# Optimization experiments

Hardware: AMD Instinct MI355X
Metric: run time of the kernel (lower is better)

## Reference

```python
import jax, jax.numpy as jnp
import numpy as np

D = 1024   # cfg.hid (downscaled from 8192)
M = 20000  # cfg.mem_c // 2 (downscaled)
B, LQ = 4, 8
PLAST_S = 0.05
IMPORTANCE = 1.0


def mha_shared_kv(q, kv_k, kv_v, Wi, bi, Wo, bo, nheads):
    """torch nn.MultiheadAttention (batch_first) with batch-shared K/V.
    q: [B,Lq,D]; kv_k/kv_v: [Lk,D] shared across batch (avoids the .repeat()
    materialization in the original torch code while computing identical math)."""
    dh = D // nheads
    Wq, Wk, Wv = jnp.split(Wi, 3, axis=0)
    bq, bk, bv = jnp.split(bi, 3)
    qp = (jnp.einsum('bqd,ed->bqe', q, Wq) + bq) * (dh ** -0.5)
    kp = kv_k @ Wk.T + bk              # [Lk,D]
    vp = kv_v @ Wv.T + bv              # [Lk,D]
    qh = qp.reshape(q.shape[0], q.shape[1], nheads, dh)      # [B,Lq,h,dh]
    kh = kp.reshape(kp.shape[0], nheads, dh)                 # [Lk,h,dh]
    vh = vp.reshape(vp.shape[0], nheads, dh)                 # [Lk,h,dh]
    scores = jnp.einsum('bqhd,khd->bhqk', qh, kh)            # [B,h,Lq,Lk]
    attn = jax.nn.softmax(scores, axis=-1)
    ctx = jnp.einsum('bhqk,khd->bqhd', attn, vh)
    ctx = ctx.reshape(q.shape[0], q.shape[1], D)
    return ctx @ Wo.T + bo


def setup_inputs() -> dict:
    key = jax.random.key(0)
    ks = jax.random.split(key, 16)
    s = 0.02
    return {
        'q':    jax.random.normal(ks[0], (B, LQ, D), jnp.float32),
        'data': jax.random.normal(ks[1], (B, D), jnp.float32),
        'ek':   jax.random.normal(ks[2], (M, D), jnp.float32),
        'ev':   jax.random.normal(ks[3], (M, D), jnp.float32),
        'sk':   jax.random.normal(ks[4], (M, D), jnp.float32),
        'sv':   jax.random.normal(ks[5], (M, D), jnp.float32),
        'wm':   jax.random.normal(ks[6], (10, D), jnp.float32),
        'Wi_e': jax.random.normal(ks[7], (3 * D, D), jnp.float32) * s,
        'bi_e': jnp.zeros((3 * D,), jnp.float32),
        'Wo_e': jax.random.normal(ks[8], (D, D), jnp.float32) * s,
        'bo_e': jnp.zeros((D,), jnp.float32),
        'Wi_s': jax.random.normal(ks[9], (3 * D, D), jnp.float32) * s,
        'bi_s': jnp.zeros((3 * D,), jnp.float32),
        'Wo_s': jax.random.normal(ks[10], (D, D), jnp.float32) * s,
        'bo_s': jnp.zeros((D,), jnp.float32),
        'Wi_w': jax.random.normal(ks[11], (3 * D, D), jnp.float32) * s,
        'bi_w': jnp.zeros((3 * D,), jnp.float32),
        'Wo_w': jax.random.normal(ks[12], (D, D), jnp.float32) * s,
        'bo_w': jnp.zeros((D,), jnp.float32),
        'Wrp':  jax.random.normal(ks[13], (D, 3 * D), jnp.float32) * s,
        'brp':  jnp.zeros((D,), jnp.float32),
        'eu':   jnp.zeros((M,), jnp.float32),
    }


def reference(q, data, ek, ev, sk, sv, wm,
              Wi_e, bi_e, Wo_e, bo_e,
              Wi_s, bi_s, Wo_s, bo_s,
              Wi_w, bi_w, Wo_w, bo_w,
              Wrp, brp, eu):
    # ---- NeuroMemory.read ----
    e_r = mha_shared_kv(q, ek, ev, Wi_e, bi_e, Wo_e, bo_e, 16)
    s_r = mha_shared_kv(q, sk, sv, Wi_s, bi_s, Wo_s, bo_s, 16)
    w_r = mha_shared_kv(q, wm, wm, Wi_w, bi_w, Wo_w, bo_w, 8)
    read_out = jnp.concatenate([e_r, s_r, w_r], axis=-1) @ Wrp.T + brp  # [B,Lq,D]

    # ---- NeuroMemory.write (episodic, Hebbian plasticity update) ----
    scores = data @ ek.T                       # [B,M]
    probs = jax.nn.softmax(scores, axis=-1)    # [B,M]
    upd = probs * (PLAST_S * IMPORTANCE)       # [B,M]
    u = upd.mean(axis=0)[:, None]              # [M,1] (batch-mean update strength)
    d = data.mean(axis=0)[None, :]             # [1,D]
    new_ek = ek * (1.0 - u) + d * u            # [M,D]
    new_ev = ev * (1.0 - u) + d * u            # [M,D]
    new_eu = eu * 0.99 + jax.lax.stop_gradient(probs.sum(axis=0))  # [M]
    return (read_out, new_ek, new_ev, new_eu)
```

## Files before the change

### kernel.cpp

```cpp
#include <hip/hip_runtime.h>
#include <hip/hip_fp16.h>
#include <hip/hip_bf16.h>
#include <cstdint>
#include <cstddef>

#define D_HID 1024
#define MEM_M 20000
#define NBATCH 4
#define BL 32
#define NROWS 512
#define SROWS_E 516
#define SROWS_S 512
#define BK 32
#define LDT 40
#define PV_NC 20

typedef __attribute__((ext_vector_type(8))) short short8;
typedef __attribute__((ext_vector_type(4))) float f32x4;
typedef __attribute__((ext_vector_type(16))) float f32x16;
typedef __attribute__((ext_vector_type(4))) unsigned short us4;

__device__ inline ushort f2bf(float f) {
    __hip_bfloat16 b = __float2bfloat16(f);
    return *reinterpret_cast<ushort*>(&b);
}
__device__ inline float h2f(ushort u) {
    __half h; *reinterpret_cast<ushort*>(&h) = u; return __half2float(h);
}

__device__ __forceinline__ void block_sync_lds() {
    asm volatile("s_waitcnt lgkmcnt(0)" ::: "memory");
    __builtin_amdgcn_s_barrier();
}

struct SkDesc  { const float* A; const float* B; int K; int M; };
struct SkDescs { SkDesc d[5]; };
struct RdDesc  { const float* bias; float* dst; int M; int ldc; float alpha; };
struct RdDescs { RdDesc d[5]; };

__device__ __forceinline__ void skinny_body(const SkDesc dd, float* __restrict__ part,
                                            int gk, int k0, int n0, int tid)
{
    __shared__ float As[32][132];
    __shared__ float Bs[64][129];
    const int K = dd.K, M = dd.M;
    {
        const int r = tid >> 3, cbl = (tid & 7) * 16;
        if (r < M) {
            const float* src = dd.A + (size_t)r * K + k0 + cbl;
            #pragma unroll
            for (int i = 0; i < 4; ++i) {
                const float4 v = *(const float4*)(src + i * 4);
                As[r][cbl + i * 4 + 0] = v.x; As[r][cbl + i * 4 + 1] = v.y;
                As[r][cbl + i * 4 + 2] = v.z; As[r][cbl + i * 4 + 3] = v.w;
            }
        } else {
            #pragma unroll
            for (int i = 0; i < 16; ++i) As[r][cbl + i] = 0.f;
        }
    }
    {
        const int r = tid >> 2, cbl = (tid & 3) * 32;
        const float* src = dd.B + (size_t)(n0 + r) * K + k0 + cbl;
        #pragma unroll
        for (int i = 0; i < 8; ++i) {
            const float4 v = *(const float4*)(src + i * 4);
            Bs[r][cbl + i * 4 + 0] = v.x; Bs[r][cbl + i * 4 + 1] = v.y;
            Bs[r][cbl + i * 4 + 2] = v.z; Bs[r][cbl + i * 4 + 3] = v.w;
        }
    }
    __syncthreads();
    const int n = tid & 63, mg = tid >> 6;
    float acc[8];
    #pragma unroll
    for (int i = 0; i < 8; ++i) acc[i] = 0.f;
    #pragma unroll 4
    for (int k = 0; k < 128; k += 4) {
        const float b0 = Bs[n][k + 0], b1 = Bs[n][k + 1];
        const float b2 = Bs[n][k + 2], b3 = Bs[n][k + 3];
        #pragma unroll
        for (int i = 0; i < 8; ++i) {
            const float4 a = *(const float4*)&As[mg * 8 + i][k];
            acc[i] = fmaf(a.x, b0, fmaf(a.y, b1, fmaf(a.z, b2, fmaf(a.w, b3, acc[i]))));
        }
    }
    #pragma unroll
    for (int i = 0; i < 8; ++i)
        part[((size_t)gk * 32 + mg * 8 + i) * 1024 + n0 + n] = acc[i];
}

__global__ __launch_bounds__(256)
void k_skinny(SkDescs ds, float* __restrict__ part)
{
    skinny_body(ds.d[blockIdx.z], part,
                blockIdx.z * gridDim.y + blockIdx.y,
                blockIdx.y * 128, blockIdx.x * 64, threadIdx.x);
}

__global__ __launch_bounds__(256)
void k_head(SkDescs ds, float* __restrict__ part,
            const float* __restrict__ ek, const float* __restrict__ sk,
            ushort* __restrict__ kvb)
{
    const int bx = blockIdx.x;
    const int tid = threadIdx.x;
    if (bx < 640) {
        const int g = bx >> 7;
        const int rem = bx & 127;
        const int kc = rem >> 4;
        const int n0 = (rem & 15) * 64;
        skinny_body(ds.d[g], part, g * 8 + kc, kc * 128, n0, tid);
    } else {
        const size_t nchunks = (size_t)2 * MEM_M * D_HID / 8;
        for (size_t i = (size_t)(bx - 640) * 256 + tid; i < nchunks;
             i += (size_t)1408 * 256) {
            const size_t base = i * 8;
            const float* src = (base < (size_t)MEM_M * D_HID)
                             ? (ek + base) : (sk + base - (size_t)MEM_M * D_HID);
            const float4 v0 = *(const float4*)(src);
            const float4 v1 = *(const float4*)(src + 4);
            alignas(16) ushort o[8];
            o[0] = f2bf(v0.x); o[1] = f2bf(v0.y); o[2] = f2bf(v0.z); o[3] = f2bf(v0.w);
            o[4] = f2bf(v1.x); o[5] = f2bf(v1.y); o[6] = f2bf(v1.z); o[7] = f2bf(v1.w);
            *(short8*)(kvb + base) = *(const short8*)o;
        }
    }
}

__global__ __launch_bounds__(256)
void k_skred(RdDescs ds, const float* __restrict__ part, int nkc)
{
    const int g = blockIdx.y;
    const int m = blockIdx.x;
    const RdDesc dd = ds.d[g];
    if (m >= dd.M) return;
    const int c = threadIdx.x * 4;
    float4 s = make_float4(0.f, 0.f, 0.f, 0.f);
    for (int kc = 0; kc < nkc; ++kc) {
        const float4 v = *(const float4*)&part[((size_t)(g * nkc + kc) * 32 + m) * 1024 + c];
        s.x += v.x; s.y += v.y; s.z += v.z; s.w += v.w;
    }
    const float4 b = *(const float4*)(dd.bias + c);
    float4 o;
    o.x = (s.x + b.x) * dd.alpha; o.y = (s.y + b.y) * dd.alpha;
    o.z = (s.z + b.z) * dd.alpha; o.w = (s.w + b.w) * dd.alpha;
    *(float4*)(dd.dst + (size_t)m * dd.ldc + c) = o;
}

__global__ __launch_bounds__(256)
void mfma_scores(const ushort* __restrict__ A_e, const ushort* __restrict__ ekb,
                 const ushort* __restrict__ A_s, const ushort* __restrict__ skb,
                 __half* __restrict__ S_e, __half* __restrict__ S_s,
                 const float* __restrict__ c0_e, const float* __restrict__ c0_s)
{
    __shared__ ushort As[2][128][LDT];
    __shared__ ushort Bs[2][128][LDT];
    const int tid = threadIdx.x;
    const int i = blockIdx.x + 9 * blockIdx.y;
    const int xcd = i & 7, idx = i >> 3;
    const int wg = (xcd < 5 ? xcd * 177 : 885 + (xcd - 5) * 176) + idx;
    const int mi = wg % 9, nbk = wg / 9;
    const int bank = (mi >= 5);
    const int m0 = (bank ? (mi - 5) : mi) * 128;
    const int n0 = nbk * 128;
    const ushort* __restrict__ A = bank ? A_s : A_e;
    const ushort* __restrict__ B = bank ? skb : ekb;
    __half* __restrict__ S = bank ? S_s : S_e;
    const float* __restrict__ c0 = bank ? c0_s : c0_e;
    const int Mreal = bank ? SROWS_S : SROWS_E;

    const int wid = tid >> 6, lane = tid & 63;
    const int wr = (wid >> 1) * 64, wc = (wid & 1) * 64;
    const int l31 = lane & 31, l2 = lane >> 5;

    const int srow = tid >> 1;
    const int ac = (tid & 1) * 16;
    int gbrow = n0 + srow; if (gbrow > MEM_M - 1) gbrow = MEM_M - 1;
    const ushort* Ap = A + (size_t)(m0 + srow) * 1024 + ac;
    const ushort* Bp = B + (size_t)gbrow * 1024 + ac;

    f32x16 acc[2][2];
    #pragma unroll
    for (int fm = 0; fm < 2; ++fm)
        #pragma unroll
        for (int fn = 0; fn < 2; ++fn)
            #pragma unroll
            for (int r = 0; r < 16; ++r) acc[fm][fn][r] = 0.f;

    auto MF = [&](int bu) {
        short8 a[2][2], b[2][2];
        #pragma unroll
        for (int f = 0; f < 2; ++f)
            #pragma unroll
            for (int kh = 0; kh < 2; ++kh) {
                a[f][kh] = *(const short8*)&As[bu][wr + f * 32 + l31][kh * 16 + l2 * 8];
                b[f][kh] = *(const short8*)&Bs[bu][wc + f * 32 + l31][kh * 16 + l2 * 8];
            }
        #pragma unroll
        for (int fm = 0; fm < 2; ++fm)
            #pragma unroll
            for (int fn = 0; fn < 2; ++fn)
                #pragma unroll
                for (int kh = 0; kh < 2; ++kh)
                    acc[fm][fn] = __builtin_amdgcn_mfma_f32_32x32x16_bf16(
                        a[fm][kh], b[fn][kh], acc[fm][fn], 0, 0, 0);
    };

    short8 a00, a01, b00, b01;
    short8 a10, a11, b10, b11;

#define SC_LOAD0(KT) { a00 = *(const short8*)(Ap + (KT)); a01 = *(const short8*)(Ap + (KT) + 8); \
                       b00 = *(const short8*)(Bp + (KT)); b01 = *(const short8*)(Bp + (KT) + 8); }
#define SC_LOAD1(KT) { a10 = *(const short8*)(Ap + (KT)); a11 = *(const short8*)(Ap + (KT) + 8); \
                       b10 = *(const short8*)(Bp + (KT)); b11 = *(const short8*)(Bp + (KT) + 8); }
#define SC_STORE0(BU) { *(short8*)&As[BU][srow][ac] = a00; *(short8*)&As[BU][srow][ac + 8] = a01; \
                        *(short8*)&Bs[BU][srow][ac] = b00; *(short8*)&Bs[BU][srow][ac + 8] = b01; }
#define SC_STORE1(BU) { *(short8*)&As[BU][srow][ac] = a10; *(short8*)&As[BU][srow][ac + 8] = a11; \
                        *(short8*)&Bs[BU][srow][ac] = b10; *(short8*)&Bs[BU][srow][ac + 8] = b11; }

    SC_LOAD0(0);
    SC_LOAD1(32);
    SC_STORE0(0);
    block_sync_lds();
    for (int it = 0; it < 16; ++it) {
        const int kt = it * 64;
        if (it < 15) SC_LOAD0(kt + 64);
        MF(0);
        SC_STORE1(1);
        block_sync_lds();
        if (it < 15) SC_LOAD1(kt + 96);
        MF(1);
        if (it < 15) SC_STORE0(0);
        block_sync_lds();
    }
#undef SC_LOAD0
#undef SC_LOAD1
#undef SC_STORE0
#undef SC_STORE1

    #pragma unroll
    for (int fm = 0; fm < 2; ++fm) {
        #pragma unroll
        for (int fn = 0; fn < 2; ++fn) {
            #pragma unroll
            for (int r = 0; r < 16; ++r) {
                const int row = m0 + wr + fm * 32 + (r & 3) + 8 * (r >> 2) + 4 * l2;
                if (row >= Mreal) continue;
                const int col = n0 + wc + fn * 32 + l31;
                if (col < MEM_M)
                    S[(size_t)row * MEM_M + col] = __float2half(acc[fm][fn][r] + c0[row]);
            }
        }
    }
}

__global__ __launch_bounds__(256, 3)
void mfma_pv(const ushort* __restrict__ P_e, const ushort* __restrict__ P_s,
             const float* __restrict__ ev, const float* __restrict__ sv,
             float* __restrict__ part)
{
    __shared__ ushort As[2][128][LDT];
    __shared__ ushort Bs[2][128][LDT];
    const int tid = threadIdx.x;
    const int z = blockIdx.z;
    const int bank = (z >= PV_NC), c = bank ? (z - PV_NC) : z;
    const ushort* __restrict__ P = bank ? P_s : P_e;
    const float* __restrict__ V = bank ? sv : ev;
    const int m0 = blockIdx.y * 128, n0 = blockIdx.x * 128;
    const int ks0 = (c * 625) / PV_NC, ks1 = ((c + 1) * 625) / PV_NC;
    const int wid = tid >> 6, lane = tid & 63;
    const int wr = (wid >> 1) * 64, wc = (wid & 1) * 64;
    const int l31 = lane & 31, l2 = lane >> 5;
    const int kb = (tid & 7) * 4, nb2 = (tid >> 3) * 4;
    const int srow = tid >> 1, ac = (tid & 1) * 16;
    const ushort* Pp = P + (size_t)(m0 + srow) * MEM_M + ac;

    f32x16 acc[2][2];
    #pragma unroll
    for (int fm = 0; fm < 2; ++fm)
        #pragma unroll
        for (int fn = 0; fn < 2; ++fn)
            #pragma unroll
            for (int r = 0; r < 16; ++r) acc[fm][fn][r] = 0.f;

    auto MF = [&](int bu) {
        short8 a[2][2], b[2][2];
        #pragma unroll
        for (int f = 0; f < 2; ++f)
            #pragma unroll
            for (int kh = 0; kh < 2; ++kh) {
                a[f][kh] = *(const short8*)&As[bu][wr + f * 32 + l31][kh * 16 + l2 * 8];
                b[f][kh] = *(const short8*)&Bs[bu][wc + f * 32 + l31][kh * 16 + l2 * 8];
            }
        #pragma unroll
        for (int fm = 0; fm < 2; ++fm)
            #pragma unroll
            for (int fn = 0; fn < 2; ++fn)
                #pragma unroll
                for (int kh = 0; kh < 2; ++kh)
                    acc[fm][fn] = __builtin_amdgcn_mfma_f32_32x32x16_bf16(
                        a[fm][kh], b[fn][kh], acc[fm][fn], 0, 0, 0);
    };

    short8 pa0, pa1;
    float4 q0[4], q1[4];

#define PV_PLOAD(T) { const int kt = (T) * 32; \
    pa0 = *(const short8*)(Pp + kt); pa1 = *(const short8*)(Pp + kt + 8); }
#define PV_VLOAD(QQ, T) { const int kt = (T) * 32; \
    QQ[0] = *(const float4*)(V + (size_t)(kt + kb + 0) * 1024 + n0 + nb2); \
    QQ[1] = *(const float4*)(V + (size_t)(kt + kb + 1) * 1024 + n0 + nb2); \
    QQ[2] = *(const float4*)(V + (size_t)(kt + kb + 2) * 1024 + n0 + nb2); \
    QQ[3] = *(const float4*)(V + (size_t)(kt + kb + 3) * 1024 + n0 + nb2); }
#define PV_STORE(BU, QQ) { \
    *(short8*)&As[BU][srow][ac] = pa0; *(short8*)&As[BU][srow][ac + 8] = pa1; \
    us4 w; \
    w.x = f2bf(QQ[0].x); w.y = f2bf(QQ[1].x); w.z = f2bf(QQ[2].x); w.w = f2bf(QQ[3].x); \
    *(us4*)&Bs[BU][nb2 + 0][kb] = w; \
    w.x = f2bf(QQ[0].y); w.y = f2bf(QQ[1].y); w.z = f2bf(QQ[2].y); w.w = f2bf(QQ[3].y); \
    *(us4*)&Bs[BU][nb2 + 1][kb] = w; \
    w.x = f2bf(QQ[0].z); w.y = f2bf(QQ[1].z); w.z = f2bf(QQ[2].z); w.w = f2bf(QQ[3].z); \
    *(us4*)&Bs[BU][nb2 + 2][kb] = w; \
    w.x = f2bf(QQ[0].w); w.y = f2bf(QQ[1].w); w.z = f2bf(QQ[2].w); w.w = f2bf(QQ[3].w); \
    *(us4*)&Bs[BU][nb2 + 3][kb] = w; }

    PV_PLOAD(ks0);
    PV_VLOAD(q0, ks0);
    PV_STORE(0, q0);
    if (ks0 + 1 < ks1) PV_VLOAD(q1, ks0 + 1);
    block_sync_lds();
    for (int t = ks0; t < ks1; t += 2) {
        if (t + 1 < ks1) PV_PLOAD(t + 1);
        if (t + 2 < ks1) PV_VLOAD(q0, t + 2);
        MF(0);
        if (t + 1 < ks1) PV_STORE(1, q1);
        block_sync_lds();
        if (t + 1 < ks1) {
            if (t + 2 < ks1) PV_PLOAD(t + 2);
            if (t + 3 < ks1) PV_VLOAD(q1, t + 3);
            MF(1);
            if (t + 2 < ks1) PV_STORE(0, q0);
            block_sync_lds();
        }
    }
#undef PV_PLOAD
#undef PV_VLOAD
#undef PV_STORE

    float* __restrict__ po = part + (size_t)z * NROWS * 1024;
    #pragma unroll
    for (int fm = 0; fm < 2; ++fm)
        #pragma unroll
        for (int fn = 0; fn < 2; ++fn)
            #pragma unroll
            for (int r = 0; r < 16; ++r) {
                const int row = m0 + wr + fm * 32 + (r & 3) + 8 * (r >> 2) + 4 * l2;
                const int col = n0 + wc + fn * 32 + l31;
                po[(size_t)row * 1024 + col] = acc[fm][fn][r];
            }
}

__global__ __launch_bounds__(256)
void k_T(const float* __restrict__ qp,
         const float* __restrict__ Wi_e, const float* __restrict__ bi_e,
         const float* __restrict__ Wi_s, const float* __restrict__ bi_s,
         ushort* __restrict__ A_e, float* __restrict__ c0_e,
         ushort* __restrict__ A_s, float* __restrict__ c0_s,
         const float* __restrict__ data, float* __restrict__ dmean)
{
    const int bq = blockIdx.x;
    const int tid = threadIdx.x;
    if (bq >= 128) {
        if (bq < 252) {
            const int row = SROWS_E + (bq - 128);
            us4 z4; z4.x = 0; z4.y = 0; z4.z = 0; z4.w = 0;
            *(us4*)(A_e + (size_t)row * 1024 + tid * 4) = z4;
        } else {
            for (int t = tid; t < D_HID; t += 256) {
                float s = 0.f;
                #pragma unroll
                for (int b = 0; b < NBATCH; ++b) s += data[b * D_HID + t];
                dmean[t] = 0.25f * s;
                #pragma unroll
                for (int b = 0; b < NBATCH; ++b)
                    A_e[(size_t)(NROWS + b) * 1024 + t] = f2bf(data[b * D_HID + t]);
            }
            if (tid < NBATCH) c0_e[NROWS + tid] = 0.f;
        }
        return;
    }
    const int bank = bq >> 6;
    const int h = (bq >> 2) & 15;
    const int q4 = bq & 3;
    const float* qpB = qp + (size_t)bank * BL * D_HID;
    const float* Wk = (bank ? Wi_s : Wi_e) + (size_t)D_HID * D_HID;
    const float* bk = (bank ? bi_s : bi_e) + D_HID;
    ushort* T  = bank ? A_s : A_e;
    float* c0 = bank ? c0_s : c0_e;

    __shared__ float qs[32][64];
    for (int i = tid; i < 32 * 64; i += 256) {
        const int r = i >> 6, j = i & 63;
        qs[r][j] = qpB[(size_t)r * D_HID + h * 64 + j];
    }
    __syncthreads();
    const int e = q4 * 256 + tid;
    float acc[32];
    #pragma unroll
    for (int r = 0; r < 32; ++r) acc[r] = 0.f;
    for (int j = 0; j < 64; ++j) {
        const float w = Wk[(size_t)(h * 64 + j) * D_HID + e];
        #pragma unroll
        for (int r = 0; r < 32; ++r) acc[r] = fmaf(qs[r][j], w, acc[r]);
    }
    #pragma unroll
    for (int r = 0; r < 32; ++r) T[(size_t)(r * 16 + h) * 1024 + e] = f2bf(acc[r]);
    if (q4 == 0 && tid < 32) {
        float s = 0.f;
        for (int j = 0; j < 64; ++j) s += qs[tid][j] * bk[h * 64 + j];
        c0[tid * 16 + h] = s;
    }
}

__global__ __launch_bounds__(256)
void k_softmax(__half* __restrict__ S_e, __half* __restrict__ S_s,
               float* __restrict__ mrow, float* __restrict__ lrow)
{
    const int row = blockIdx.x;
    ushort* p = (row < SROWS_E) ? (ushort*)(S_e + (size_t)row * MEM_M)
                                : (ushort*)(S_s + (size_t)(row - SROWS_E) * MEM_M);
    const bool conv = (row < SROWS_E) ? (row < NROWS) : true;
    __shared__ float red_m[256];
    __shared__ float red_l[256];
    const int tid = threadIdx.x;
    float m = -3.0e38f, l = 0.f;
    for (int c = tid; c < MEM_M / 8; c += 256) {
        alignas(16) ushort t[8];
        *(short8*)t = *(const short8*)(p + c * 8);
        float v[8];
        #pragma unroll
        for (int j = 0; j < 8; ++j) v[j] = h2f(t[j]);
        float cm = v[0];
        #pragma unroll
        for (int j = 1; j < 8; ++j) cm = fmaxf(cm, v[j]);
        const float nm = fmaxf(m, cm);
        float s = 0.f;
        #pragma unroll
        for (int j = 0; j < 8; ++j) s += __expf(v[j] - nm);
        l = l * __expf(m - nm) + s;
        m = nm;
    }
    red_m[tid] = m; red_l[tid] = l; __syncthreads();
    for (int s = 128; s > 0; s >>= 1) {
        if (tid < s) {
            const float m2 = fmaxf(red_m[tid], red_m[tid + s]);
            red_l[tid] = red_l[tid] * __expf(red_m[tid] - m2)
                       + red_l[tid + s] * __expf(red_m[tid + s] - m2);
            red_m[tid] = m2;
        }
        __syncthreads();
    }
    const float rm = red_m[0];
    if (conv) {
        for (int c = tid; c < MEM_M / 8; c += 256) {
            alignas(16) ushort t[8];
            *(short8*)t = *(const short8*)(p + c * 8);
            alignas(16) ushort o[8];
            #pragma unroll
            for (int j = 0; j < 8; ++j) o[j] = f2bf(__expf(h2f(t[j]) - rm));
            *(short8*)(p + c * 8) = *(const short8*)o;
        }
    }
    if (tid == 0) { mrow[row] = rm; lrow[row] = red_l[0]; }
}

__global__ __launch_bounds__(256)
void k_uk(const __half* __restrict__ S_e,
          const float* __restrict__ mrow, const float* __restrict__ lrow,
          const float* __restrict__ eu,
          float* __restrict__ u, float* __restrict__ out_eu)
{
    const int k = blockIdx.x * 256 + threadIdx.x;
    if (k >= MEM_M) return;
    float sp = 0.f;
    #pragma unroll
    for (int b = 0; b < NBATCH; ++b) {
        const int row = NROWS + b;
        sp += __expf(__half2float(S_e[(size_t)row * MEM_M + k]) - mrow[row]) / lrow[row];
    }
    u[k] = 0.05f * 0.25f * sp;
    out_eu[k] = eu[k] * 0.99f + sp;
}

__global__ __launch_bounds__(256)
void k_pvred_upd(const float* __restrict__ part, const float* __restrict__ lrow,
                 float* __restrict__ R,
                 const float* __restrict__ ev, const float* __restrict__ u,
                 const float* __restrict__ dmean, float* __restrict__ out_ev)
{
    const int tid = threadIdx.x;
    if (blockIdx.x < 1024) {
        const size_t perb4 = (size_t)NROWS * 1024 / 4;
        const size_t i = (size_t)blockIdx.x * 256 + tid;
        const int bank = i >= perb4;
        const size_t off4 = i - (size_t)bank * perb4;
        const int m = (int)(off4 >> 8);
        const float inv = 1.f / lrow[bank ? (SROWS_E + m) : m];
        const float4* p = (const float4*)part + (size_t)bank * PV_NC * perb4 + off4;
        float4 s = make_float4(0.f, 0.f, 0.f, 0.f);
        #pragma unroll
        for (int c = 0; c < PV_NC; ++c) {
            const float4 v = p[(size_t)c * perb4];
            s.x += v.x; s.y += v.y; s.z += v.z; s.w += v.w;
        }
        s.x *= inv; s.y *= inv; s.z *= inv; s.w *= inv;
        ((float4*)R)[i] = s;
    } else {
        const int bid = blockIdx.x - 1024;
        const size_t n4 = (size_t)MEM_M * D_HID / 4;
        for (size_t i = (size_t)bid * 256 + tid; i < n4; i += (size_t)1024 * 256) {
            const int k = (int)(i >> 8);
            const int c = (int)(i & 255);
            const float uk = u[k];
            const float om = 1.f - uk;
            const float4 dd = ((const float4*)dmean)[c];
            const float4 b = ((const float4*)ev)[i];
            float4 ob;
            ob.x = b.x * om + dd.x * uk; ob.y = b.y * om + dd.y * uk;
            ob.z = b.z * om + dd.z * uk; ob.w = b.w * om + dd.w * uk;
            ((float4*)out_ev)[i] = ob;
        }
    }
}

__global__ __launch_bounds__(256)
void k_tail(const float* __restrict__ R,
            const float* __restrict__ Wi_e, const float* __restrict__ bi_e,
            const float* __restrict__ Wi_s, const float* __restrict__ bi_s,
            float* __restrict__ ctx,
            const float* __restrict__ qp, const float* __restrict__ kpw,
            const float* __restrict__ vpw,
            const float* __restrict__ ek, const float* __restrict__ u,
            const float* __restrict__ dmean, float* __restrict__ out_ek)
{
    __shared__ float sm[12384];
    const int tid = threadIdx.x;
    const int bx = blockIdx.x;
    if (bx < 32) {
        const int bank = bx >> 4;
        const int h = bx & 15;
        const float* Rb = R + (size_t)bank * NROWS * D_HID;
        const float* Wv = (bank ? Wi_s : Wi_e) + (size_t)2 * D_HID * D_HID;
        const float* bv = (bank ? bi_s : bi_e) + 2 * D_HID;
        float* cb = ctx + (size_t)bank * BL * D_HID;
        float (*Rs)[129] = (float(*)[129])sm;
        float (*Ws)[129] = (float(*)[129])(sm + 32 * 129);
        const int j = tid & 63;
        const int g = tid >> 6;
        float acc[8];
        #pragma unroll
        for (int i = 0; i < 8; ++i) acc[i] = 0.f;
        for (int ec = 0; ec < D_HID; ec += 128) {
            for (int i = tid; i < 32 * 128; i += 256) {
                const int r = i >> 7, e = i & 127;
                Rs[r][e] = Rb[(size_t)(r * 16 + h) * D_HID + ec + e];
            }
            for (int i = tid; i < 64 * 128; i += 256) {
                const int r = i >> 7, e = i & 127;
                Ws[r][e] = Wv[(size_t)(h * 64 + r) * D_HID + ec + e];
            }
            __syncthreads();
            for (int e = 0; e < 128; ++e) {
                const float w = Ws[j][e];
                #pragma unroll
                for (int i = 0; i < 8; ++i)
                    acc[i] = fmaf(Rs[g + 4 * i][e], w, acc[i]);
            }
            __syncthreads();
        }
        #pragma unroll
        for (int i = 0; i < 8; ++i) {
            const int bl = g + 4 * i;
            cb[(size_t)bl * D_HID + h * 64 + j] = acc[i] + bv[h * 64 + j];
        }
    } else if (bx < 64) {
        const int bl = bx - 32;
        float* q = sm;
        float (*kp)[1024] = (float(*)[1024])(sm + 1024);
        float (*pp)[10] = (float(*)[10])(sm + 1024 + 10240);
        const float* qrow = qp + (size_t)(2 * BL + bl) * D_HID;
        for (int i = tid; i < D_HID; i += 256) q[i] = qrow[i];
        for (int i = tid; i < 10 * D_HID; i += 256) kp[i >> 10][i & 1023] = kpw[i];
        __syncthreads();
        if (tid < 80) {
            const int h = tid / 10, k = tid % 10;
            float s = 0.f;
            for (int jj = 0; jj < 128; ++jj) s += q[h * 128 + jj] * kp[k][h * 128 + jj];
            pp[h][k] = s;
        }
        __syncthreads();
        if (tid < 8) {
            float m = -3.0e38f;
            for (int k = 0; k < 10; ++k) m = fmaxf(m, pp[tid][k]);
            float e[10]; float l = 0.f;
            for (int k = 0; k < 10; ++k) { e[k] = __expf(pp[tid][k] - m); l += e[k]; }
            const float inv = 1.f / l;
            for (int k = 0; k < 10; ++k) pp[tid][k] = e[k] * inv;
        }
        __syncthreads();
        float* cw = ctx + (size_t)(2 * BL + bl) * D_HID;
        for (int f = tid; f < D_HID; f += 256) {
            const int h = f >> 7;
            float s = 0.f;
            #pragma unroll
            for (int k = 0; k < 10; ++k) s += pp[h][k] * vpw[(size_t)k * D_HID + f];
            cw[f] = s;
        }
    } else {
        const int bid = bx - 64;
        const size_t n4 = (size_t)MEM_M * D_HID / 4;
        for (size_t i = (size_t)bid * 256 + tid; i < n4; i += (size_t)1024 * 256) {
            const int k = (int)(i >> 8);
            const int c = (int)(i & 255);
            const float uk = u[k];
            const float om = 1.f - uk;
            const float4 dd = ((const float4*)dmean)[c];
            const float4 a = ((const float4*)ek)[i];
            float4 oa;
            oa.x = a.x * om + dd.x * uk; oa.y = a.y * om + dd.y * uk;
            oa.z = a.z * om + dd.z * uk; oa.w = a.w * om + dd.w * uk;
            ((float4*)out_ek)[i] = oa;
        }
    }
}

extern "C" void kernel_launch(void* const* d_in, const int* in_sizes, int n_in,
                              void* d_out, int out_size, void* d_ws, size_t ws_size,
                              hipStream_t stream)
{
    (void)in_sizes; (void)n_in; (void)out_size; (void)ws_size;
    const float* q    = (const float*)d_in[0];
    const float* data = (const float*)d_in[1];
    const float* ek   = (const float*)d_in[2];
    const float* ev   = (const float*)d_in[3];
    const float* sk   = (const float*)d_in[4];
    const float* sv   = (const float*)d_in[5];
    const float* wm   = (const float*)d_in[6];
    const float* Wi_e = (const float*)d_in[7];
    const float* bi_e = (const float*)d_in[8];
    const float* Wo_e = (const float*)d_in[9];
    const float* bo_e = (const float*)d_in[10];
    const float* Wi_s = (const float*)d_in[11];
    const float* bi_s = (const float*)d_in[12];
    const float* Wo_s = (const float*)d_in[13];
    const float* bo_s = (const float*)d_in[14];
    const float* Wi_w = (const float*)d_in[15];
    const float* bi_w = (const float*)d_in[16];
    const float* Wo_w = (const float*)d_in[17];
    const float* bo_w = (const float*)d_in[18];
    const float* Wrp  = (const float*)d_in[19];
    const float* brp  = (const float*)d_in[20];
    const float* eu   = (const float*)d_in[21];

    float* out = (float*)d_out;
    float* out_read = out;
    float* out_ek = out + 32768;
    float* out_ev = out_ek + 20480000;
    float* out_eu = out_ev + 20480000;

    float* ws    = (float*)d_ws;
    float* qp    = ws;
    float* A_e   = qp + 98304;
    float* A_s   = A_e + 655360;
    float* c0_e  = A_s + 524288;
    float* c0_s  = c0_e + 640;
    float* dmean = c0_s + 512;
    float* u     = dmean + 1024;
    float* mrow  = u + 20480;
    float* lrow  = mrow + 1032;
    float* kpw   = lrow + 1032;
    float* vpw   = kpw + 10240;
    float* ctx   = vpw + 10240;
    float* cat   = ctx + 98304;
    float* skpart = cat + 98304;
    float* Rbuf  = skpart;

    ushort* A_e16 = (ushort*)A_e;
    ushort* A_s16 = (ushort*)A_s;

    ushort* ekb = (ushort*)out_ek;
    ushort* skb = ekb + (size_t)MEM_M * D_HID;
    float* part = out_ek;
    __half* S_e = (__half*)out_ev;
    __half* S_s = S_e + (size_t)SROWS_E * MEM_M;

    const dim3 b256(256);
    const float sc16 = 0.125f;
    const float sc8  = 0.08838834764831845f;

    SkDescs s1;
    s1.d[0] = {q,  Wi_e,            1024, 32};
    s1.d[1] = {q,  Wi_s,            1024, 32};
    s1.d[2] = {q,  Wi_w,            1024, 32};
    s1.d[3] = {wm, Wi_w + 1048576,  1024, 10};
    s1.d[4] = {wm, Wi_w + 2097152,  1024, 10};
    k_head<<<2048, b256, 0, stream>>>(s1, skpart, ek, sk, ekb);
    RdDescs r1;
    r1.d[0] = {bi_e,        qp,         32, 1024, sc16};
    r1.d[1] = {bi_s,        qp + 32768, 32, 1024, sc16};
    r1.d[2] = {bi_w,        qp + 65536, 32, 1024, sc8};
    r1.d[3] = {bi_w + 1024, kpw,        10, 1024, 1.f};
    r1.d[4] = {bi_w + 2048, vpw,        10, 1024, 1.f};
    k_skred<<<dim3(32, 5), b256, 0, stream>>>(r1, skpart, 8);

    k_T<<<253, b256, 0, stream>>>(qp, Wi_e, bi_e, Wi_s, bi_s,
                                  A_e16, c0_e, A_s16, c0_s, data, dmean);

    mfma_scores<<<dim3(9, 157), b256, 0, stream>>>(A_e16, ekb, A_s16, skb,
                                                   S_e, S_s, c0_e, c0_s);

    k_softmax<<<SROWS_E + SROWS_S, b256, 0, stream>>>(S_e, S_s, mrow, lrow);
    k_uk<<<79, b256, 0, stream>>>(S_e, mrow, lrow, eu, u, out_eu);

    mfma_pv<<<dim3(8, 4, 2 * PV_NC), b256, 0, stream>>>(
        (const ushort*)S_e, (const ushort*)S_s, ev, sv, part);

    k_pvred_upd<<<2048, b256, 0, stream>>>(part, lrow, Rbuf, ev, u, dmean, out_ev);

    k_tail<<<1088, b256, 0, stream>>>(Rbuf, Wi_e, bi_e, Wi_s, bi_s, ctx,
                                      qp, kpw, vpw, ek, u, dmean, out_ek);

    SkDescs s2;
    s2.d[0] = {ctx,         Wo_e, 1024, 32};
    s2.d[1] = {ctx + 32768, Wo_s, 1024, 32};
    s2.d[2] = {ctx + 65536, Wo_w, 1024, 32};
    s2.d[3] = {ctx,         Wo_e, 1024, 32};
    s2.d[4] = {ctx,         Wo_e, 1024, 32};
    k_skinny<<<dim3(16, 8, 3), b256, 0, stream>>>(s2, skpart);
    RdDescs r2;
    r2.d[0] = {bo_e, cat,        32, 3072, 1.f};
    r2.d[1] = {bo_s, cat + 1024, 32, 3072, 1.f};
    r2.d[2] = {bo_w, cat + 2048, 32, 3072, 1.f};
    r2.d[3] = r2.d[0];
    r2.d[4] = r2.d[0];
    k_skred<<<dim3(32, 3), b256, 0, stream>>>(r2, skpart, 8);

    SkDescs s3;
    s3.d[0] = {cat, Wrp, 3072, 32};
    s3.d[1] = s3.d[0]; s3.d[2] = s3.d[0]; s3.d[3] = s3.d[0]; s3.d[4] = s3.d[0];
    k_skinny<<<dim3(16, 24, 1), b256, 0, stream>>>(s3, skpart);
    RdDescs r3;
    r3.d[0] = {brp, out_read, 32, 1024, 1.f};
    r3.d[1] = r3.d[0]; r3.d[2] = r3.d[0]; r3.d[3] = r3.d[0]; r3.d[4] = r3.d[0];
    k_skred<<<dim3(32, 1), b256, 0, stream>>>(r3, skpart, 24);
}
```

Baseline: 500.0 us.

## Load P fragments directly into registers and deepen V pipeline in PV GEMM

The PV kernel now reads P (already bf16) straight from global memory into MFMA operand registers instead of staging it through LDS. V tiles are quad-buffered in LDS and processed two k-steps per barrier, which halves the barrier count. Blocks are remapped with a swizzled index for better L2 locality, the split-K count drops from 20 to 16, and the occupancy hint is removed. The trade-off is more registers and less coalesced P loads, since each lane reads a 16-byte piece of a different row.

```diff
diff --git a/kernel.cpp b/kernel.cpp
--- a/kernel.cpp
+++ b/kernel.cpp
@@ -13,7 +13,7 @@
 #define SROWS_S 512
 #define BK 32
 #define LDT 40
-#define PV_NC 20
+#define PV_NC 16
 
 typedef __attribute__((ext_vector_type(8))) short short8;
 typedef __attribute__((ext_vector_type(4))) float f32x4;
@@ -254,26 +254,28 @@
     }
 }
 
-__global__ __launch_bounds__(256, 3)
+__global__ __launch_bounds__(256)
 void mfma_pv(const ushort* __restrict__ P_e, const ushort* __restrict__ P_s,
              const float* __restrict__ ev, const float* __restrict__ sv,
              float* __restrict__ part)
 {
-    __shared__ ushort As[2][128][LDT];
-    __shared__ ushort Bs[2][128][LDT];
+    __shared__ ushort Bs[4][128][LDT];
     const int tid = threadIdx.x;
-    const int z = blockIdx.z;
-    const int bank = (z >= PV_NC), c = bank ? (z - PV_NC) : z;
+    const int bid = blockIdx.x + 8 * (blockIdx.y + 4 * blockIdx.z);
+    const int wgs = (bid & 7) * 128 + (bid >> 3);
+    const int nI = wgs & 7, mI = (wgs >> 3) & 3;
+    const int z = wgs >> 5;
+    const int bank = z >> 4, c = z & 15;
     const ushort* __restrict__ P = bank ? P_s : P_e;
     const float* __restrict__ V = bank ? sv : ev;
-    const int m0 = blockIdx.y * 128, n0 = blockIdx.x * 128;
+    const int m0 = mI * 128, n0 = nI * 128;
     const int ks0 = (c * 625) / PV_NC, ks1 = ((c + 1) * 625) / PV_NC;
     const int wid = tid >> 6, lane = tid & 63;
     const int wr = (wid >> 1) * 64, wc = (wid & 1) * 64;
     const int l31 = lane & 31, l2 = lane >> 5;
     const int kb = (tid & 7) * 4, nb2 = (tid >> 3) * 4;
-    const int srow = tid >> 1, ac = (tid & 1) * 16;
-    const ushort* Pp = P + (size_t)(m0 + srow) * MEM_M + ac;
+    const ushort* Pp0 = P + (size_t)(m0 + wr + l31) * MEM_M + l2 * 8;
+    const ushort* Pp1 = P + (size_t)(m0 + wr + 32 + l31) * MEM_M + l2 * 8;
 
     f32x16 acc[2][2];
     #pragma unroll
@@ -283,15 +285,49 @@
             #pragma unroll
             for (int r = 0; r < 16; ++r) acc[fm][fn][r] = 0.f;
 
-    auto MF = [&](int bu) {
-        short8 a[2][2], b[2][2];
+    short8 P0[2][2], P1[2][2];
+    float4 q0[4], q1[4];
+
+    auto PLOAD0 = [&](int T) {
+        const int kt = T * 32;
+        #pragma unroll
+        for (int kh = 0; kh < 2; ++kh) {
+            P0[0][kh] = *(const short8*)(Pp0 + kt + kh * 16);
+            P0[1][kh] = *(const short8*)(Pp1 + kt + kh * 16);
+        }
+    };
+    auto PLOAD1 = [&](int T) {
+        const int kt = T * 32;
+        #pragma unroll
+        for (int kh = 0; kh < 2; ++kh) {
+            P1[0][kh] = *(const short8*)(Pp0 + kt + kh * 16);
+            P1[1][kh] = *(const short8*)(Pp1 + kt + kh * 16);
+        }
+    };
+    auto VLOAD = [&](float4* qq, int T) {
+        const int kt = T * 32;
+        #pragma unroll
+        for (int r = 0; r < 4; ++r)
+            qq[r] = *(const float4*)(V + (size_t)(kt + kb + r) * 1024 + n0 + nb2);
+    };
+    auto VSTORE = [&](int BU, const float4* qq) {
+        us4 w;
+        w.x = f2bf(qq[0].x); w.y = f2bf(qq[1].x); w.z = f2bf(qq[2].x); w.w = f2bf(qq[3].x);
+        *(us4*)&Bs[BU][nb2 + 0][kb] = w;
+        w.x = f2bf(qq[0].y); w.y = f2bf(qq[1].y); w.z = f2bf(qq[2].y); w.w = f2bf(qq[3].y);
+        *(us4*)&Bs[BU][nb2 + 1][kb] = w;
+        w.x = f2bf(qq[0].z); w.y = f2bf(qq[1].z); w.z = f2bf(qq[2].z); w.w = f2bf(qq[3].z);
+        *(us4*)&Bs[BU][nb2 + 2][kb] = w;
+        w.x = f2bf(qq[0].w); w.y = f2bf(qq[1].w); w.z = f2bf(qq[2].w); w.w = f2bf(qq[3].w);
+        *(us4*)&Bs[BU][nb2 + 3][kb] = w;
+    };
+    auto MF = [&](const short8 pa[2][2], int bu) {
+        short8 b[2][2];
         #pragma unroll
         for (int f = 0; f < 2; ++f)
             #pragma unroll
-            for (int kh = 0; kh < 2; ++kh) {
-                a[f][kh] = *(const short8*)&As[bu][wr + f * 32 + l31][kh * 16 + l2 * 8];
+            for (int kh = 0; kh < 2; ++kh)
                 b[f][kh] = *(const short8*)&Bs[bu][wc + f * 32 + l31][kh * 16 + l2 * 8];
-            }
         #pragma unroll
         for (int fm = 0; fm < 2; ++fm)
             #pragma unroll
@@ -299,53 +335,28 @@
                 #pragma unroll
                 for (int kh = 0; kh < 2; ++kh)
                     acc[fm][fn] = __builtin_amdgcn_mfma_f32_32x32x16_bf16(
-                        a[fm][kh], b[fn][kh], acc[fm][fn], 0, 0, 0);
+                        pa[fm][kh], b[fn][kh], acc[fm][fn], 0, 0, 0);
     };
 
-    short8 pa0, pa1;
-    float4 q0[4], q1[4];
-
-#define PV_PLOAD(T) { const int kt = (T) * 32; \
-    pa0 = *(const short8*)(Pp + kt); pa1 = *(const short8*)(Pp + kt + 8); }
-#define PV_VLOAD(QQ, T) { const int kt = (T) * 32; \
-    QQ[0] = *(const float4*)(V + (size_t)(kt + kb + 0) * 1024 + n0 + nb2); \
-    QQ[1] = *(const float4*)(V + (size_t)(kt + kb + 1) * 1024 + n0 + nb2); \
-    QQ[2] = *(const float4*)(V + (size_t)(kt + kb + 2) * 1024 + n0 + nb2); \
-    QQ[3] = *(const float4*)(V + (size_t)(kt + kb + 3) * 1024 + n0 + nb2); }
-#define PV_STORE(BU, QQ) { \
-    *(short8*)&As[BU][srow][ac] = pa0; *(short8*)&As[BU][srow][ac + 8] = pa1; \
-    us4 w; \
-    w.x = f2bf(QQ[0].x); w.y = f2bf(QQ[1].x); w.z = f2bf(QQ[2].x); w.w = f2bf(QQ[3].x); \
-    *(us4*)&Bs[BU][nb2 + 0][kb] = w; \
-    w.x = f2bf(QQ[0].y); w.y = f2bf(QQ[1].y); w.z = f2bf(QQ[2].y); w.w = f2bf(QQ[3].y); \
-    *(us4*)&Bs[BU][nb2 + 1][kb] = w; \
-    w.x = f2bf(QQ[0].z); w.y = f2bf(QQ[1].z); w.z = f2bf(QQ[2].z); w.w = f2bf(QQ[3].z); \
-    *(us4*)&Bs[BU][nb2 + 2][kb] = w; \
-    w.x = f2bf(QQ[0].w); w.y = f2bf(QQ[1].w); w.z = f2bf(QQ[2].w); w.w = f2bf(QQ[3].w); \
-    *(us4*)&Bs[BU][nb2 + 3][kb] = w; }
-
-    PV_PLOAD(ks0);
-    PV_VLOAD(q0, ks0);
-    PV_STORE(0, q0);
-    if (ks0 + 1 < ks1) PV_VLOAD(q1, ks0 + 1);
+    PLOAD0(ks0); PLOAD1(ks0 + 1);
+    VLOAD(q0, ks0); VLOAD(q1, ks0 + 1);
+    VSTORE(0, q0); VSTORE(1, q1);
+    VLOAD(q0, ks0 + 2); VLOAD(q1, ks0 + 3);
     block_sync_lds();
+
     for (int t = ks0; t < ks1; t += 2) {
-        if (t + 1 < ks1) PV_PLOAD(t + 1);
-        if (t + 2 < ks1) PV_VLOAD(q0, t + 2);
-        MF(0);
-        if (t + 1 < ks1) PV_STORE(1, q1);
+        const int cur = (((t - ks0) >> 1) & 1) * 2;
+        const int nxt = cur ^ 2;
+        if (t + 2 < ks1) VSTORE(nxt, q0);
+        if (t + 3 < ks1) VSTORE(nxt + 1, q1);
+        if (t + 4 < ks1) VLOAD(q0, t + 4);
+        if (t + 5 < ks1) VLOAD(q1, t + 5);
+        MF(P0, cur);
+        if (t + 1 < ks1) MF(P1, cur + 1);
+        if (t + 2 < ks1) PLOAD0(t + 2);
+        if (t + 3 < ks1) PLOAD1(t + 3);
         block_sync_lds();
-        if (t + 1 < ks1) {
-            if (t + 2 < ks1) PV_PLOAD(t + 2);
-            if (t + 3 < ks1) PV_VLOAD(q1, t + 3);
-            MF(1);
-            if (t + 2 < ks1) PV_STORE(0, q0);
-            block_sync_lds();
-        }
-    }
-#undef PV_PLOAD
-#undef PV_VLOAD
-#undef PV_STORE
+    }
 
     float* __restrict__ po = part + (size_t)z * NROWS * 1024;
     #pragma unroll
```

After: 493.0 us. Within noise of the previous version (-1.4%).
